# Kernel tuning notes

Measured on AMD Instinct MI355X. Metric: run time of the kernel, lower is better.

Reference implementation:

```python
import jax, jax.numpy as jnp
import numpy as np

N = 50000      # nodes
E = 800000     # edges (before self loops)
D = 128        # embedding_dimension
HEADS = 4
C = 32         # hidden_channels
NEG_SLOPE = 0.2


def setup_inputs() -> dict:
    key = jax.random.key(0)
    ks = jax.random.split(key, 12)
    s = 0.1
    x = jax.random.normal(ks[0], (N, D), jnp.float32)
    edge_index = jax.random.randint(ks[1], (2, E), 0, N)
    # layer 1: D -> HEADS*C, concat
    W1 = jax.random.normal(ks[2], (D, HEADS * C), jnp.float32) * s
    a_src1 = jax.random.normal(ks[3], (HEADS, C), jnp.float32) * s
    a_dst1 = jax.random.normal(ks[4], (HEADS, C), jnp.float32) * s
    b1 = jnp.zeros((HEADS * C,), jnp.float32)
    # layer 2: HEADS*C -> HEADS*C, concat
    W2 = jax.random.normal(ks[5], (HEADS * C, HEADS * C), jnp.float32) * s
    a_src2 = jax.random.normal(ks[6], (HEADS, C), jnp.float32) * s
    a_dst2 = jax.random.normal(ks[7], (HEADS, C), jnp.float32) * s
    b2 = jnp.zeros((HEADS * C,), jnp.float32)
    # layer 3: HEADS*C -> C, heads=1, no concat (mean over the single head)
    W3 = jax.random.normal(ks[8], (HEADS * C, C), jnp.float32) * s
    a_src3 = jax.random.normal(ks[9], (1, C), jnp.float32) * s
    a_dst3 = jax.random.normal(ks[10], (1, C), jnp.float32) * s
    b3 = jnp.zeros((C,), jnp.float32)
    return {"x": x, "edge_index": edge_index,
            "W1": W1, "a_src1": a_src1, "a_dst1": a_dst1, "b1": b1,
            "W2": W2, "a_src2": a_src2, "a_dst2": a_dst2, "b2": b2,
            "W3": W3, "a_src3": a_src3, "a_dst3": a_dst3, "b3": b3}


def gat_layer(x, src, dst, W, a_s, a_d, b, heads, concat):
    """One PyG-style GATConv (eval mode: dropout inactive).
    x: [N, Fin]; src/dst: [E2] (self loops included)."""
    n = x.shape[0]
    h = (x @ W).reshape(n, heads, -1)                 # [N, H, C]
    alpha_src = (h * a_s).sum(-1)                     # [N, H]
    alpha_dst = (h * a_d).sum(-1)                     # [N, H]
    logits = jax.nn.leaky_relu(alpha_src[src] + alpha_dst[dst], NEG_SLOPE)  # [E2, H]
    # segment softmax over destination nodes
    m = jax.ops.segment_max(logits, dst, num_segments=n)          # [N, H]
    ex = jnp.exp(logits - m[dst])                                  # [E2, H]
    denom = jax.ops.segment_sum(ex, dst, num_segments=n)          # [N, H]
    alpha = ex / (denom[dst] + 1e-16)                              # [E2, H]
    msg = h[src] * alpha[:, :, None]                               # [E2, H, C]
    out = jax.ops.segment_sum(msg, dst, num_segments=n)            # [N, H, C]
    if concat:
        return out.reshape(n, -1) + b
    return out.mean(axis=1) + b


def reference(x, edge_index, W1, a_src1, a_dst1, b1, W2, a_src2, a_dst2, b2,
              W3, a_src3, a_dst3, b3):
    loops = jnp.arange(N, dtype=edge_index.dtype)
    src = jnp.concatenate([edge_index[0], loops])   # add_self_loops=True
    dst = jnp.concatenate([edge_index[1], loops])
    h = gat_layer(x, src, dst, W1, a_src1, a_dst1, b1, HEADS, True)
    h = jax.nn.elu(h)
    h = gat_layer(h, src, dst, W2, a_src2, a_dst2, b2, HEADS, True)
    h = jax.nn.elu(h)
    out = gat_layer(h, src, dst, W3, a_src3, a_dst3, b3, 1, False)
    return out
```

## Files before the change

### kernel.cpp

```cpp
#include <hip/hip_runtime.h>
#include <cmath>

constexpr int NN  = 50000;
constexpr int EE  = 800000;
constexpr int E2C = EE + NN;

constexpr int NBUCK = 256;
constexpr int BW    = 196;
constexpr int EPT   = 8;
constexpr int CH    = 256 * EPT;
constexpr int NB_B  = (E2C + CH - 1) / CH;
constexpr int CAP   = 4096;
constexpr int SCAP  = 5120;
constexpr int G1ALL = (NN + 63) / 64;
constexpr int G1A   = 391;

using bf16x8 = __attribute__((ext_vector_type(8))) short;
using f32x4  = __attribute__((ext_vector_type(4))) float;

__device__ inline unsigned bf16rne(float f) {
    unsigned u = __builtin_bit_cast(unsigned, f);
    return (u + 0x7fffu + ((u >> 16) & 1u)) >> 16;
}
__device__ inline float bflo(unsigned u) { return __builtin_bit_cast(float, u << 16); }
__device__ inline float bfhi(unsigned u) { return __builtin_bit_cast(float, u & 0xffff0000u); }

__global__ __launch_bounds__(256) void cvt_weights(
    const float* __restrict__ W1, const float* __restrict__ W2,
    const float* __restrict__ W3,
    unsigned short* __restrict__ W1t, unsigned short* __restrict__ W2t,
    unsigned short* __restrict__ W3t, int* __restrict__ bcursor,
    float* __restrict__ AS1, float* __restrict__ AS2, float* __restrict__ AS3,
    unsigned short* __restrict__ H1, unsigned short* __restrict__ H2,
    unsigned short* __restrict__ H3)
{
    int g = blockIdx.x * 256 + threadIdx.x;
    if (g < NBUCK) bcursor[g] = 0;
    if (g < 4) { AS1[NN * 4 + g] = -1e30f; AS2[NN * 4 + g] = -1e30f; }
    if (g == 4) AS3[NN] = -1e30f;
    if (g < 128) { H1[(size_t)NN * 128 + g] = 0; H2[(size_t)NN * 128 + g] = 0; }
    if (g < 32)  H3[(size_t)NN * 32 + g] = 0;

    const float* W; unsigned short* Wt; int cols;
    if (g < 2048)      { W = W1; Wt = W1t; cols = 128; }
    else if (g < 4096) { W = W2; Wt = W2t; cols = 128; g -= 2048; }
    else if (g < 4608) { W = W3; Wt = W3t; cols = 32;  g -= 4096; }
    else return;
    int c  = g / 16;
    int k8 = (g % 16) * 8;
    unsigned up[4];
    #pragma unroll
    for (int j = 0; j < 4; ++j) {
        float a = W[(k8 + 2 * j) * cols + c];
        float b = W[(k8 + 2 * j + 1) * cols + c];
        up[j] = bf16rne(a) | (bf16rne(b) << 16);
    }
    uint4 u; u.x = up[0]; u.y = up[1]; u.z = up[2]; u.w = up[3];
    *(uint4*)(Wt + c * 128 + k8) = u;
}

template<int NT, int NH, bool F32IN>
__device__ inline void gemm_body(
    int bid, const void* __restrict__ inv, const unsigned short* __restrict__ Wt,
    const float* __restrict__ a_s, const float* __restrict__ a_d,
    unsigned short* __restrict__ hout, float* __restrict__ asrc,
    float* __restrict__ adst)
{
    constexpr int COLS = NT * 16;
    constexpr int TPH  = NT / NH;
    const int lane = threadIdx.x & 63;
    const int wave = threadIdx.x >> 6;
    const int m    = lane & 15;
    const int quad = lane >> 4;
    const int n0   = bid * 64 + wave * 16;

    int arow = n0 + m; if (arow >= NN) arow = NN - 1;

    f32x4 acc[NT] = {};
    #pragma unroll
    for (int kq = 0; kq < 4; ++kq) {
        bf16x8 a;
        if constexpr (F32IN) {
            const float* ap = (const float*)inv + (long long)arow * 128 + quad * 8 + kq * 32;
            float4 v0 = *(const float4*)ap;
            float4 v1 = *(const float4*)(ap + 4);
            a[0] = (short)bf16rne(v0.x); a[1] = (short)bf16rne(v0.y);
            a[2] = (short)bf16rne(v0.z); a[3] = (short)bf16rne(v0.w);
            a[4] = (short)bf16rne(v1.x); a[5] = (short)bf16rne(v1.y);
            a[6] = (short)bf16rne(v1.z); a[7] = (short)bf16rne(v1.w);
        } else {
            a = *(const bf16x8*)((const unsigned short*)inv
                    + (long long)arow * 128 + quad * 8 + kq * 32);
        }
        #pragma unroll
        for (int t = 0; t < NT; ++t) {
            bf16x8 b = *(const bf16x8*)(Wt + (t * 16 + m) * 128 + kq * 32 + quad * 8);
            acc[t] = __builtin_amdgcn_mfma_f32_16x16x32_bf16(a, b, acc[t], 0, 0, 0);
        }
    }

    #pragma unroll
    for (int r = 0; r < 4; ++r) {
        int node = n0 + quad * 4 + r;
        if (node < NN) {
            #pragma unroll
            for (int t = 0; t < NT; ++t)
                hout[(long long)node * COLS + t * 16 + m] =
                    (unsigned short)bf16rne(acc[t][r]);
        }
    }

    float asv[NT], adv[NT];
    #pragma unroll
    for (int t = 0; t < NT; ++t) { asv[t] = a_s[t * 16 + m]; adv[t] = a_d[t * 16 + m]; }

    #pragma unroll
    for (int r = 0; r < 4; ++r) {
        const int node = n0 + quad * 4 + r;
        #pragma unroll
        for (int hh = 0; hh < NH; ++hh) {
            float ps = 0.f, pd = 0.f;
            #pragma unroll
            for (int q = 0; q < TPH; ++q) {
                int t = hh * TPH + q;
                ps = fmaf(acc[t][r], asv[t], ps);
                pd = fmaf(acc[t][r], adv[t], pd);
            }
            #pragma unroll
            for (int off = 8; off > 0; off >>= 1) {
                ps += __shfl_down(ps, off, 16);
                pd += __shfl_down(pd, off, 16);
            }
            if (m == 0 && node < NN) {
                asrc[node * NH + hh] = ps;
                adst[node * NH + hh] = pd;
            }
        }
    }
}

__device__ inline void bin_body(
    int bid, const int* __restrict__ ei, int* __restrict__ bcursor,
    unsigned* __restrict__ pairs)
{
    __shared__ int cnt[NBUCK];
    __shared__ int scanex[NBUCK];
    __shared__ int base[NBUCK];
    __shared__ int cur[NBUCK];
    __shared__ unsigned stage[CH];

    const int tid = threadIdx.x;
    const long long e0 = (long long)bid * CH;
    cnt[tid] = 0;
    __syncthreads();

    unsigned rec[EPT]; int bk[EPT];
    #pragma unroll
    for (int j = 0; j < EPT; ++j) {
        long long e = e0 + tid + j * 256;
        bool valid = e < E2C;
        int ss = 0, dd = 0;
        if (valid) {
            if (e < EE) { ss = ei[e]; dd = ei[EE + e]; }
            else        { ss = dd = (int)(e - EE); }
        }
        int b = dd / BW;
        bk[j]  = valid ? b : -1;
        rec[j] = (unsigned)ss | ((unsigned)(dd - b * BW) << 16) | ((unsigned)b << 24);
        if (valid) atomicAdd(&cnt[b], 1);
    }
    __syncthreads();

    const int myc = cnt[tid];
    scanex[tid] = myc;
    __syncthreads();
    for (int off = 1; off < NBUCK; off <<= 1) {
        int t = (tid >= off) ? scanex[tid - off] : 0;
        __syncthreads();
        scanex[tid] += t;
        __syncthreads();
    }
    int excl = scanex[tid] - myc;
    __syncthreads();
    scanex[tid] = excl;
    cur[tid]    = excl;
    base[tid]   = atomicAdd(&bcursor[tid], myc);
    __syncthreads();

    #pragma unroll
    for (int j = 0; j < EPT; ++j) {
        if (bk[j] >= 0) {
            int p = atomicAdd(&cur[bk[j]], 1);
            stage[p] = rec[j];
        }
    }
    __syncthreads();

    const int total = (e0 + CH <= E2C) ? CH : (int)(E2C - e0);
    for (int j = tid; j < total; j += 256) {
        unsigned p = stage[j];
        int b = (int)(p >> 24);
        pairs[(size_t)b * CAP + base[b] + (j - scanex[b])] = p;
    }
}

__device__ inline void sort_body(
    int b, const int* __restrict__ bcursor, const unsigned* __restrict__ pairs,
    int2* __restrict__ rowp, unsigned short* __restrict__ sorted_src)
{
    __shared__ int deg[256];
    __shared__ int scn[256];
    __shared__ int cur[256];
    const int n0 = b * BW;
    const int n1 = (n0 + BW < NN) ? n0 + BW : NN;
    const int nloc = n1 - n0;
    const int tid = threadIdx.x;
    const int mycnt = bcursor[b];
    const unsigned* seg = pairs + (size_t)b * CAP;
    const int base = b * SCAP;

    deg[tid] = 0;
    __syncthreads();
    for (int i = tid; i < mycnt; i += 256)
        atomicAdd(&deg[(seg[i] >> 16) & 0xff], 1);
    __syncthreads();

    const int pv = (deg[tid] + 3) & ~3;
    scn[tid] = pv;
    __syncthreads();
    for (int off = 1; off < 256; off <<= 1) {
        int t = (tid >= off) ? scn[tid - off] : 0;
        __syncthreads();
        scn[tid] += t;
        __syncthreads();
    }
    const int totalp = scn[255];
    const int pexcl  = scn[tid] - pv;
    cur[tid] = base + pexcl;
    if (tid < nloc) rowp[n0 + tid] = make_int2(base + pexcl, base + pexcl + pv);
    __syncthreads();

    int lim = totalp + 8; if (lim > SCAP) lim = SCAP;
    for (int i = tid; i < lim; i += 256)
        sorted_src[base + i] = (unsigned short)NN;
    if (b == NBUCK - 1 && tid < 8)
        sorted_src[NBUCK * SCAP + tid] = (unsigned short)NN;
    __syncthreads();
    for (int i = tid; i < mycnt; i += 256) {
        unsigned p = seg[i];
        int pos = atomicAdd(&cur[(p >> 16) & 0xff], 1);
        sorted_src[pos] = (unsigned short)(p & 0xffff);
    }
}

__global__ __launch_bounds__(256) void bin_gemm(
    const int* __restrict__ ei, int* __restrict__ bcursor,
    unsigned* __restrict__ pairs,
    const float* __restrict__ x, const unsigned short* __restrict__ Wt,
    const float* __restrict__ a_s, const float* __restrict__ a_d,
    unsigned short* __restrict__ hout, float* __restrict__ asrc,
    float* __restrict__ adst)
{
    if (blockIdx.x < NB_B)
        bin_body(blockIdx.x, ei, bcursor, pairs);
    else
        gemm_body<8, 4, true>(blockIdx.x - NB_B, x, Wt, a_s, a_d, hout, asrc, adst);
}

__global__ __launch_bounds__(256) void sort_gemm(
    const int* __restrict__ bcursor, const unsigned* __restrict__ pairs,
    int2* __restrict__ rowp, unsigned short* __restrict__ sorted_src,
    const float* __restrict__ x, const unsigned short* __restrict__ Wt,
    const float* __restrict__ a_s, const float* __restrict__ a_d,
    unsigned short* __restrict__ hout, float* __restrict__ asrc,
    float* __restrict__ adst)
{
    if (blockIdx.x < NBUCK)
        sort_body(blockIdx.x, bcursor, pairs, rowp, sorted_src);
    else
        gemm_body<8, 4, true>(blockIdx.x - NBUCK + G1A, x, Wt, a_s, a_d,
                              hout, asrc, adst);
}

template<int COLS, int NH, bool DO_ELU>
__device__ inline void aggr_node(
    int d, int lc,
    const int2* __restrict__ rowp, const unsigned short* __restrict__ sorted_src,
    const unsigned short* __restrict__ hin,
    const float* __restrict__ asrc, const float* __restrict__ adst,
    const float* __restrict__ bias, float v[8])
{
    constexpr int USTR = COLS / 2;
    const int cc = lc * 8;
    const int head = cc / 32;
    const float ad = adst[d * NH + head];
    const int2 be = rowp[d];
    const int beg = be.x, end = be.y;
    const uint* hp = (const uint*)hin + cc / 2;

    float num[8] = {};
    float den = 0.f;

    ushort4 sv = *(const ushort4*)&sorted_src[beg];
    for (int i = beg; i < end; i += 4) {
        ushort4 nx = *(const ushort4*)&sorted_src[i + 4];
        const int s[4] = {sv.x, sv.y, sv.z, sv.w};
        float a[4];
        uint4 Hv[4];
        #pragma unroll
        for (int j = 0; j < 4; ++j) a[j] = asrc[s[j] * NH + head];
        #pragma unroll
        for (int j = 0; j < 4; ++j)
            Hv[j] = *(const uint4*)&hp[(long long)s[j] * USTR];
        #pragma unroll
        for (int j = 0; j < 4; ++j) {
            float l = a[j] + ad; l = l > 0.f ? l : 0.2f * l;
            float w = __builtin_expf(l);
            den += w;
            num[0] = fmaf(w, bflo(Hv[j].x), num[0]); num[1] = fmaf(w, bfhi(Hv[j].x), num[1]);
            num[2] = fmaf(w, bflo(Hv[j].y), num[2]); num[3] = fmaf(w, bfhi(Hv[j].y), num[3]);
            num[4] = fmaf(w, bflo(Hv[j].z), num[4]); num[5] = fmaf(w, bfhi(Hv[j].z), num[5]);
            num[6] = fmaf(w, bflo(Hv[j].w), num[6]); num[7] = fmaf(w, bfhi(Hv[j].w), num[7]);
        }
        sv = nx;
    }

    float inv = 1.f / (den + 1e-16f);
    #pragma unroll
    for (int j = 0; j < 8; ++j) {
        v[j] = num[j] * inv + bias[cc + j];
        if (DO_ELU) v[j] = v[j] > 0.f ? v[j] : expm1f(v[j]);
    }
}

template<int NT_OUT, int NH_OUT>
__global__ __launch_bounds__(256) void aggr_gemm(
    const int2* __restrict__ rowp, const unsigned short* __restrict__ sorted_src,
    const unsigned short* __restrict__ hin,
    const float* __restrict__ asrc_in, const float* __restrict__ adst_in,
    const float* __restrict__ bias,
    const unsigned short* __restrict__ Wt,
    const float* __restrict__ a_s, const float* __restrict__ a_d,
    unsigned short* __restrict__ hout, float* __restrict__ asrc_out,
    float* __restrict__ adst_out)
{
    __shared__ unsigned short lds_h[16 * 128];
    const int tid = threadIdx.x;
    const int row = tid / 16;
    const int lc  = tid % 16;
    const int d   = blockIdx.x * 16 + row;

    float v[8];
    aggr_node<128, 4, true>(d, lc, rowp, sorted_src, hin, asrc_in, adst_in,
                            bias, v);

    uint4 u;
    u.x = bf16rne(v[0]) | (bf16rne(v[1]) << 16);
    u.y = bf16rne(v[2]) | (bf16rne(v[3]) << 16);
    u.z = bf16rne(v[4]) | (bf16rne(v[5]) << 16);
    u.w = bf16rne(v[6]) | (bf16rne(v[7]) << 16);
    *(uint4*)((char*)lds_h + row * 256 + ((lc * 16) ^ ((row & 7) << 4))) = u;
    __syncthreads();

    const int lane = tid & 63;
    const int wave = tid >> 6;
    const int m    = lane & 15;
    const int quad = lane >> 4;
    int t0;
    if constexpr (NT_OUT == 8) t0 = wave * 2;
    else { if (wave != 0) return; t0 = 0; }

    f32x4 acc[2] = {};
    #pragma unroll
    for (int kq = 0; kq < 4; ++kq) {
        int colb = (quad * 16 + kq * 64) ^ ((m & 7) << 4);
        bf16x8 a = *(const bf16x8*)((const char*)lds_h + m * 256 + colb);
        #pragma unroll
        for (int tt = 0; tt < 2; ++tt) {
            bf16x8 b = *(const bf16x8*)(Wt + ((t0 + tt) * 16 + m) * 128
                                        + kq * 32 + quad * 8);
            acc[tt] = __builtin_amdgcn_mfma_f32_16x16x32_bf16(a, b, acc[tt], 0, 0, 0);
        }
    }

    constexpr int COLS_OUT = NT_OUT * 16;
    const int head = t0 / (NT_OUT / NH_OUT);
    const int n0   = blockIdx.x * 16;
    float asv[2], adv[2];
    #pragma unroll
    for (int tt = 0; tt < 2; ++tt) {
        asv[tt] = a_s[(t0 + tt) * 16 + m];
        adv[tt] = a_d[(t0 + tt) * 16 + m];
    }

    #pragma unroll
    for (int r = 0; r < 4; ++r) {
        const int node = n0 + quad * 4 + r;
        #pragma unroll
        for (int tt = 0; tt < 2; ++tt)
            hout[(long long)node * COLS_OUT + (t0 + tt) * 16 + m] =
                (unsigned short)bf16rne(acc[tt][r]);
        float ps = acc[0][r] * asv[0];
        ps = fmaf(acc[1][r], asv[1], ps);
        float pd = acc[0][r] * adv[0];
        pd = fmaf(acc[1][r], adv[1], pd);
        #pragma unroll
        for (int off = 8; off > 0; off >>= 1) {
            ps += __shfl_down(ps, off, 16);
            pd += __shfl_down(pd, off, 16);
        }
        if (m == 0) {
            asrc_out[node * NH_OUT + head] = ps;
            adst_out[node * NH_OUT + head] = pd;
        }
    }
}

template<int COLS, int NH>
__global__ __launch_bounds__(256) void aggr_final(
    const int2* __restrict__ rowp, const unsigned short* __restrict__ sorted_src,
    const unsigned short* __restrict__ hin,
    const float* __restrict__ asrc, const float* __restrict__ adst,
    const float* __restrict__ bias, float* __restrict__ out)
{
    constexpr int TPN = COLS / 8;
    int t = blockIdx.x * 256 + threadIdx.x;
    int d = t / TPN;
    int lc = t % TPN;
    if (d >= NN) return;
    float v[8];
    aggr_node<COLS, NH, false>(d, lc, rowp, sorted_src, hin, asrc, adst, bias, v);
    float4 o0 = {v[0], v[1], v[2], v[3]};
    float4 o1 = {v[4], v[5], v[6], v[7]};
    *(float4*)&out[(long long)d * COLS + lc * 8]     = o0;
    *(float4*)&out[(long long)d * COLS + lc * 8 + 4] = o1;
}

extern "C" void kernel_launch(void* const* d_in, const int* in_sizes, int n_in,
                              void* d_out, int out_size, void* d_ws, size_t ws_size,
                              hipStream_t stream)
{
    const float* x   = (const float*)d_in[0];
    const int*   ei  = (const int*)  d_in[1];
    const float* W1  = (const float*)d_in[2];
    const float* as1 = (const float*)d_in[3];
    const float* ad1 = (const float*)d_in[4];
    const float* b1  = (const float*)d_in[5];
    const float* W2  = (const float*)d_in[6];
    const float* as2 = (const float*)d_in[7];
    const float* ad2 = (const float*)d_in[8];
    const float* b2  = (const float*)d_in[9];
    const float* W3  = (const float*)d_in[10];
    const float* as3 = (const float*)d_in[11];
    const float* ad3 = (const float*)d_in[12];
    const float* b3  = (const float*)d_in[13];
    float* out = (float*)d_out;

    unsigned short* H1  = (unsigned short*)d_ws;
    unsigned short* H2  = H1 + (size_t)(NN + 1) * 128;
    unsigned short* H3  = H2 + (size_t)(NN + 1) * 128;
    unsigned short* W1t = H3 + (size_t)(NN + 1) * 32;
    unsigned short* W2t = W1t + 128 * 128;
    unsigned short* W3t = W2t + 128 * 128;
    float* AS1 = (float*)(W3t + 32 * 128);
    float* AD1 = AS1 + (size_t)(NN + 1) * 4;
    float* AS2 = AD1 + (size_t)NN * 4;
    float* AD2 = AS2 + (size_t)(NN + 1) * 4;
    float* AS3 = AD2 + (size_t)NN * 4;
    float* AD3 = AS3 + (size_t)(NN + 1);
    int2* rowp = (int2*)(AD3 + NN);
    unsigned short* sorted = (unsigned short*)(rowp + NN);
    int* bcursor = (int*)(sorted + (size_t)NBUCK * SCAP + 8);
    size_t off = ((size_t)(bcursor + NBUCK) - (size_t)d_ws + 15) & ~(size_t)15;
    unsigned* pairs = (unsigned*)((char*)d_ws + off);

    const int gCvtW  = (4608 + 255) / 256;
    const int gBinG  = NB_B + G1A;
    const int gSortG = NBUCK + (G1ALL - G1A);
    const int gFused = NN / 16;
    const int gAggr3 = (NN * 4 + 255) / 256;

    cvt_weights<<<gCvtW, 256, 0, stream>>>(W1, W2, W3, W1t, W2t, W3t, bcursor,
                                           AS1, AS2, AS3, H1, H2, H3);
    bin_gemm<<<gBinG, 256, 0, stream>>>(ei, bcursor, pairs,
                                        x, W1t, as1, ad1, H1, AS1, AD1);
    sort_gemm<<<gSortG, 256, 0, stream>>>(bcursor, pairs, rowp, sorted,
                                          x, W1t, as1, ad1, H1, AS1, AD1);
    aggr_gemm<8, 4><<<gFused, 256, 0, stream>>>(
        rowp, sorted, H1, AS1, AD1, b1, W2t, as2, ad2, H2, AS2, AD2);
    aggr_gemm<2, 1><<<gFused, 256, 0, stream>>>(
        rowp, sorted, H2, AS2, AD2, b2, W3t, as3, ad3, H3, AS3, AD3);
    aggr_final<32, 1><<<gAggr3, 256, 0, stream>>>(
        rowp, sorted, H3, AS3, AD3, b3, out);
}
```

Before: 258.5 us.

## Sort nodes by degree within buckets so aggregation blocks have balanced work

```diff
diff --git a/kernel.cpp b/kernel.cpp
--- a/kernel.cpp
+++ b/kernel.cpp
@@ -206,11 +206,15 @@
 
 __device__ inline void sort_body(
     int b, const int* __restrict__ bcursor, const unsigned* __restrict__ pairs,
-    int2* __restrict__ rowp, unsigned short* __restrict__ sorted_src)
+    int2* __restrict__ rowp, unsigned short* __restrict__ sorted_src,
+    unsigned short* __restrict__ perm)
 {
     __shared__ int deg[256];
     __shared__ int scn[256];
     __shared__ int cur[256];
+    __shared__ int hist2[64];
+    __shared__ int scn2[64];
+    __shared__ int cur2[64];
     const int n0 = b * BW;
     const int n1 = (n0 + BW < NN) ? n0 + BW : NN;
     const int nloc = n1 - n0;
@@ -220,13 +224,16 @@
     const int base = b * SCAP;
 
     deg[tid] = 0;
+    if (tid < 64) hist2[tid] = 0;
     __syncthreads();
     for (int i = tid; i < mycnt; i += 256)
         atomicAdd(&deg[(seg[i] >> 16) & 0xff], 1);
     __syncthreads();
 
     const int pv = (deg[tid] + 3) & ~3;
+    int it = pv >> 2; if (it > 63) it = 63;
     scn[tid] = pv;
+    if (tid < nloc) atomicAdd(&hist2[it], 1);
     __syncthreads();
     for (int off = 1; off < 256; off <<= 1) {
         int t = (tid >= off) ? scn[tid - off] : 0;
@@ -234,10 +241,25 @@
         scn[tid] += t;
         __syncthreads();
     }
+    if (tid < 64) scn2[tid] = hist2[tid];
+    __syncthreads();
+    for (int off = 1; off < 64; off <<= 1) {
+        int t = (tid >= off && tid < 64) ? scn2[tid - off] : 0;
+        __syncthreads();
+        if (tid < 64) scn2[tid] += t;
+        __syncthreads();
+    }
+    if (tid < 64) cur2[tid] = scn2[tid] - hist2[tid];
+    __syncthreads();
+
     const int totalp = scn[255];
     const int pexcl  = scn[tid] - pv;
     cur[tid] = base + pexcl;
-    if (tid < nloc) rowp[n0 + tid] = make_int2(base + pexcl, base + pexcl + pv);
+    if (tid < nloc) {
+        int rank = atomicAdd(&cur2[it], 1);
+        perm[n0 + rank] = (unsigned short)(n0 + tid);
+        rowp[n0 + rank] = make_int2(base + pexcl, base + pexcl + pv);
+    }
     __syncthreads();
 
     int lim = totalp + 8; if (lim > SCAP) lim = SCAP;
@@ -270,13 +292,14 @@
 __global__ __launch_bounds__(256) void sort_gemm(
     const int* __restrict__ bcursor, const unsigned* __restrict__ pairs,
     int2* __restrict__ rowp, unsigned short* __restrict__ sorted_src,
+    unsigned short* __restrict__ perm,
     const float* __restrict__ x, const unsigned short* __restrict__ Wt,
     const float* __restrict__ a_s, const float* __restrict__ a_d,
     unsigned short* __restrict__ hout, float* __restrict__ asrc,
     float* __restrict__ adst)
 {
     if (blockIdx.x < NBUCK)
-        sort_body(blockIdx.x, bcursor, pairs, rowp, sorted_src);
+        sort_body(blockIdx.x, bcursor, pairs, rowp, sorted_src, perm);
     else
         gemm_body<8, 4, true>(blockIdx.x - NBUCK + G1A, x, Wt, a_s, a_d,
                               hout, asrc, adst);
@@ -284,7 +307,7 @@
 
 template<int COLS, int NH, bool DO_ELU>
 __device__ inline void aggr_node(
-    int d, int lc,
+    int d, int rk, int lc,
     const int2* __restrict__ rowp, const unsigned short* __restrict__ sorted_src,
     const unsigned short* __restrict__ hin,
     const float* __restrict__ asrc, const float* __restrict__ adst,
@@ -294,7 +317,7 @@
     const int cc = lc * 8;
     const int head = cc / 32;
     const float ad = adst[d * NH + head];
-    const int2 be = rowp[d];
+    const int2 be = rowp[rk];
     const int beg = be.x, end = be.y;
     const uint* hp = (const uint*)hin + cc / 2;
 
@@ -335,6 +358,7 @@
 
 template<int NT_OUT, int NH_OUT>
 __global__ __launch_bounds__(256) void aggr_gemm(
+    const unsigned short* __restrict__ perm,
     const int2* __restrict__ rowp, const unsigned short* __restrict__ sorted_src,
     const unsigned short* __restrict__ hin,
     const float* __restrict__ asrc_in, const float* __restrict__ adst_in,
@@ -345,13 +369,16 @@
     float* __restrict__ adst_out)
 {
     __shared__ unsigned short lds_h[16 * 128];
+    __shared__ int lds_node[16];
     const int tid = threadIdx.x;
     const int row = tid / 16;
     const int lc  = tid % 16;
-    const int d   = blockIdx.x * 16 + row;
+    const int rk  = blockIdx.x * 16 + row;
+    const int d   = perm[rk];
+    if (lc == 0) lds_node[row] = d;
 
     float v[8];
-    aggr_node<128, 4, true>(d, lc, rowp, sorted_src, hin, asrc_in, adst_in,
+    aggr_node<128, 4, true>(d, rk, lc, rowp, sorted_src, hin, asrc_in, adst_in,
                             bias, v);
 
     uint4 u;
@@ -385,7 +412,6 @@
 
     constexpr int COLS_OUT = NT_OUT * 16;
     const int head = t0 / (NT_OUT / NH_OUT);
-    const int n0   = blockIdx.x * 16;
     float asv[2], adv[2];
     #pragma unroll
     for (int tt = 0; tt < 2; ++tt) {
@@ -395,7 +421,7 @@
 
     #pragma unroll
     for (int r = 0; r < 4; ++r) {
-        const int node = n0 + quad * 4 + r;
+        const int node = lds_node[quad * 4 + r];
         #pragma unroll
         for (int tt = 0; tt < 2; ++tt)
             hout[(long long)node * COLS_OUT + (t0 + tt) * 16 + m] =
@@ -418,6 +444,7 @@
 
 template<int COLS, int NH>
 __global__ __launch_bounds__(256) void aggr_final(
+    const unsigned short* __restrict__ perm,
     const int2* __restrict__ rowp, const unsigned short* __restrict__ sorted_src,
     const unsigned short* __restrict__ hin,
     const float* __restrict__ asrc, const float* __restrict__ adst,
@@ -425,11 +452,13 @@
 {
     constexpr int TPN = COLS / 8;
     int t = blockIdx.x * 256 + threadIdx.x;
-    int d = t / TPN;
+    int rk = t / TPN;
     int lc = t % TPN;
-    if (d >= NN) return;
+    if (rk >= NN) return;
+    const int d = perm[rk];
     float v[8];
-    aggr_node<COLS, NH, false>(d, lc, rowp, sorted_src, hin, asrc, adst, bias, v);
+    aggr_node<COLS, NH, false>(d, rk, lc, rowp, sorted_src, hin, asrc, adst,
+                               bias, v);
     float4 o0 = {v[0], v[1], v[2], v[3]};
     float4 o1 = {v[4], v[5], v[6], v[7]};
     *(float4*)&out[(long long)d * COLS + lc * 8]     = o0;
@@ -471,7 +500,8 @@
     int2* rowp = (int2*)(AD3 + NN);
     unsigned short* sorted = (unsigned short*)(rowp + NN);
     int* bcursor = (int*)(sorted + (size_t)NBUCK * SCAP + 8);
-    size_t off = ((size_t)(bcursor + NBUCK) - (size_t)d_ws + 15) & ~(size_t)15;
+    unsigned short* perm = (unsigned short*)(bcursor + NBUCK);
+    size_t off = ((size_t)(perm + NN) - (size_t)d_ws + 15) & ~(size_t)15;
     unsigned* pairs = (unsigned*)((char*)d_ws + off);
 
     const int gCvtW  = (4608 + 255) / 256;
@@ -484,12 +514,12 @@
                                            AS1, AS2, AS3, H1, H2, H3);
     bin_gemm<<<gBinG, 256, 0, stream>>>(ei, bcursor, pairs,
                                         x, W1t, as1, ad1, H1, AS1, AD1);
-    sort_gemm<<<gSortG, 256, 0, stream>>>(bcursor, pairs, rowp, sorted,
+    sort_gemm<<<gSortG, 256, 0, stream>>>(bcursor, pairs, rowp, sorted, perm,
                                           x, W1t, as1, ad1, H1, AS1, AD1);
     aggr_gemm<8, 4><<<gFused, 256, 0, stream>>>(
-        rowp, sorted, H1, AS1, AD1, b1, W2t, as2, ad2, H2, AS2, AD2);
+        perm, rowp, sorted, H1, AS1, AD1, b1, W2t, as2, ad2, H2, AS2, AD2);
     aggr_gemm<2, 1><<<gFused, 256, 0, stream>>>(
-        rowp, sorted, H2, AS2, AD2, b2, W3t, as3, ad3, H3, AS3, AD3);
+        perm, rowp, sorted, H2, AS2, AD2, b2, W3t, as3, ad3, H3, AS3, AD3);
     aggr_final<32, 1><<<gAggr3, 256, 0, stream>>>(
-        rowp, sorted, H3, AS3, AD3, b3, out);
-}
+        perm, rowp, sorted, H3, AS3, AD3, b3, out);
+}
```

New measurement: 256.8 us. About the same (-0.6%).
